# Kernel optimization log

Measured on AMD Instinct MI355X. Metric: run time of the kernel, lower is better.

## Reference

```python
import jax, jax.numpy as jnp
import numpy as np

BETA = 0.25
EPS = 1e-12

def setup_inputs() -> dict:
    key = jax.random.key(0)
    k1, k2 = jax.random.split(key)
    f_BChw = jax.random.normal(k1, (32, 64, 32, 32), dtype=jnp.float32)
    emb_weight = jax.random.normal(k2, (8192, 64), dtype=jnp.float32)
    return {"f_BChw": f_BChw, "emb_weight": emb_weight}

def reference(f_BChw, emb_weight):
    f = f_BChw.astype(jnp.float32)
    B, C, h, w = f.shape
    V = emb_weight.shape[0]
    # flatten tokens: [B,C,h,w] -> [N,C]
    NxC = jnp.transpose(f, (0, 2, 3, 1)).reshape(-1, C)
    # cosine nearest-neighbor on detached, L2-normalized queries/codes
    q = jax.lax.stop_gradient(NxC)
    q = q / jnp.maximum(jnp.linalg.norm(q, axis=-1, keepdims=True), EPS)
    wn = emb_weight / jnp.maximum(jnp.linalg.norm(emb_weight, axis=-1, keepdims=True), EPS)
    sim = q @ wn.T                      # [N,V] -- dominant memory traffic
    idx_N = jnp.argmax(sim, axis=1)     # [N]
    # gather codes -> [B,C,h,w]
    fhat = emb_weight[idx_N].reshape(B, h, w, C).transpose(0, 3, 1, 2)
    sg = jax.lax.stop_gradient
    vq_loss = BETA * jnp.mean((sg(fhat) - f) ** 2) + jnp.mean((fhat - sg(f)) ** 2)
    # straight-through estimator
    fhat_out = f + sg(fhat - f)
    # usage statistics (bincount)
    counts = jnp.zeros((V,), jnp.float32).at[idx_N].add(1.0)
    prob = counts / counts.sum()
    vocab_usage = jnp.mean((prob > 0.01 / V).astype(jnp.float32)) * 100.0
    entropy_loss = jnp.float32(0.0)
    return fhat_out, vq_loss, entropy_loss, vocab_usage
```

## Files before the change

kernel.cpp:

```cpp
#include <hip/hip_runtime.h>

typedef _Float16 f16x8 __attribute__((ext_vector_type(8)));
typedef float f32x16 __attribute__((ext_vector_type(16)));

#define V_TOTAL 8192
#define C_DIM   64
#define N_TOK   32768
#define INV2048 4.8828125e-4f
#define THR_COEF 2.2e-3f

#define VSPLIT1 4
#define VSEG1   2048
#define CH1     32
#define VSPLIT2 8
#define VSEG2   1024
#define CH2     32

typedef const __attribute__((address_space(1))) _Float16 glb_f16;
typedef __attribute__((address_space(3))) _Float16 lds_f16;


__device__ __forceinline__ unsigned long long packkey(float s, int idx) {
    unsigned u = __float_as_uint(s);
    unsigned k = u ^ ((unsigned)(((int)u) >> 31) | 0x80000000u);
    return ((unsigned long long)k << 32) | (unsigned)(8191 - idx);
}

__global__ __launch_bounds__(256)
void k_prep(const float* __restrict__ w, _Float16* __restrict__ cp,
            unsigned long long* __restrict__ keys, int* __restrict__ counts,
            int* __restrict__ unc_cnt) {
    int v = blockIdx.x * 256 + threadIdx.x;
    counts[v] = 0;
    if (v == 0) unc_cnt[0] = 0;
#pragma unroll
    for (int i = 0; i < 4; ++i) keys[v * 4 + i] = 0ull;
    const float4* row = (const float4*)(w + v * C_DIM);
    float4 r[16];
    float s = 0.f;
#pragma unroll
    for (int i = 0; i < 16; ++i) {
        r[i] = row[i];
        s += r[i].x * r[i].x + r[i].y * r[i].y + r[i].z * r[i].z + r[i].w * r[i].w;
    }
    float inv = 1.0f / fmaxf(sqrtf(s), 1e-12f);
    const float* rs = (const float*)r;
    const int cv = v >> 5, c = v & 31;
#pragma unroll
    for (int q = 0; q < 8; ++q) {
        f16x8 hi, lo;
#pragma unroll
        for (int j = 0; j < 8; ++j) {
            float x = rs[q * 8 + j] * inv;
            _Float16 h = (_Float16)x;
            hi[j] = h;
            lo[j] = (_Float16)((x - (float)h) * 2048.0f);
        }
        *(f16x8*)(cp + cv * 4096 +        q * 256 + c * 8) = hi;
        *(f16x8*)(cp + cv * 4096 + 2048 + q * 256 + c * 8) = lo;
    }
}

__global__ __launch_bounds__(256, 4)
void k_pass1(const float* __restrict__ f, const _Float16* __restrict__ cp,
             float* __restrict__ m1s, float* __restrict__ m2s,
             int* __restrict__ i1s, float* __restrict__ fn2) {
    __shared__ __align__(16) _Float16 lds[4][4096];

    const int tid  = threadIdx.x;
    const int lane = tid & 63;
    const int wid  = tid >> 6;
    const int c31  = lane & 31;
    const int g    = lane >> 5;
    const int seg  = blockIdx.y;
    const int t0   = blockIdx.x * 128 + wid * 32;

    f16x8 bh[4];
    float s2 = 0.f;
    {
        const int T = t0 + c31;
        const float* fb = f + (T >> 10) * 65536 + (T & 1023);
#pragma unroll
        for (int ks = 0; ks < 4; ++ks) {
#pragma unroll
            for (int j = 0; j < 8; ++j) {
                float v = fb[(ks * 16 + g * 8 + j) * 1024];
                s2 += v * v;
                bh[ks][j] = (_Float16)v;
            }
        }
    }

    const _Float16* seg_cp = cp + (size_t)seg * (VSEG1 / 32) * 4096;

    auto stage = [&](int cv) {
        const _Float16* s0 = seg_cp + (2 * cv + 0) * 4096 + wid * 512 + lane * 8;
        const _Float16* s1 = seg_cp + (2 * cv + 1) * 4096 + wid * 512 + lane * 8;
        _Float16* d0 = &lds[cv & 3][wid * 512];
        _Float16* d1 = &lds[cv & 3][2048 + wid * 512];
        __builtin_amdgcn_global_load_lds((glb_f16*)s0, (lds_f16*)d0, 16, 0, 0);
        __builtin_amdgcn_global_load_lds((glb_f16*)s1, (lds_f16*)d1, 16, 0, 0);
    };

    const f32x16 zacc = {0.f,0.f,0.f,0.f,0.f,0.f,0.f,0.f,0.f,0.f,0.f,0.f,0.f,0.f,0.f,0.f};

    float m1 = -3.4e38f, m2 = -3.4e38f;
    int   i1 = 0;

    stage(0); stage(1); stage(2);

#pragma unroll 1
    for (int cv = 0; cv < CH1; ++cv) {
        if (cv < CH1 - 2)       asm volatile("s_waitcnt vmcnt(4)" ::: "memory");
        else if (cv == CH1 - 2) asm volatile("s_waitcnt vmcnt(2)" ::: "memory");
        else                    asm volatile("s_waitcnt vmcnt(0)" ::: "memory");
        __builtin_amdgcn_s_barrier();
        if (cv + 3 < CH1) stage(cv + 3);

        const _Float16* base = &lds[cv & 3][g * 256 + c31 * 8];
#pragma unroll
        for (int tile = 0; tile < 2; ++tile) {
            const _Float16* tb = base + tile * 2048;
            f16x8 A0 = *(const f16x8*)(tb);
            f16x8 A1 = *(const f16x8*)(tb + 512);
            f16x8 A2 = *(const f16x8*)(tb + 1024);
            f16x8 A3 = *(const f16x8*)(tb + 1536);
            f32x16 amA, amB;
            amA = __builtin_amdgcn_mfma_f32_32x32x16_f16(A0, bh[0], zacc, 0, 0, 0);
            amB = __builtin_amdgcn_mfma_f32_32x32x16_f16(A2, bh[2], zacc, 0, 0, 0);
            amA = __builtin_amdgcn_mfma_f32_32x32x16_f16(A1, bh[1], amA, 0, 0, 0);
            amB = __builtin_amdgcn_mfma_f32_32x32x16_f16(A3, bh[3], amB, 0, 0, 0);

            const int codebase = seg * VSEG1 + cv * 64 + tile * 32;
#pragma unroll
            for (int r = 0; r < 16; ++r) {
                const int codeq = codebase + (r & 3) + 8 * (r >> 2);
                float s = amA[r] + amB[r];
                float nm2 = __builtin_amdgcn_fmed3f(m1, m2, s);
                bool u = s > m1;
                i1 = u ? codeq : i1;
                m1 = fmaxf(m1, s);
                m2 = nm2;
            }
        }
    }

    i1 += 4 * g;
    {
        float om1 = __shfl_xor(m1, 32);
        float om2 = __shfl_xor(m2, 32);
        int   oi1 = __shfl_xor(i1, 32);
        float nm2 = fmaxf(fminf(m1, om1), fmaxf(m2, om2));
        bool rep = om1 > m1;
        i1 = rep ? oi1 : i1;
        m1 = fmaxf(m1, om1);
        m2 = nm2;
        float os2 = __shfl_xor(s2, 32);
        s2 += os2;
    }
    if (lane < 32) {
        const int t = t0 + c31;
        m1s[seg * N_TOK + t] = m1;
        m2s[seg * N_TOK + t] = m2;
        i1s[seg * N_TOK + t] = i1;
        fn2[t] = s2;
    }
}

__global__ __launch_bounds__(256)
void k_classify(const float* __restrict__ m1s, const float* __restrict__ m2s,
                const int* __restrict__ i1s, const float* __restrict__ fn2,
                int* __restrict__ idxf, int* __restrict__ unc_list,
                int* __restrict__ unc_cnt) {
    const int t = blockIdx.x * 256 + threadIdx.x;
    float a1 = m1s[t], a2 = m2s[t];
    int   ai = i1s[t];
#pragma unroll
    for (int s = 1; s < VSPLIT1; ++s) {
        float b1 = m1s[s * N_TOK + t];
        float b2 = m2s[s * N_TOK + t];
        int   bi = i1s[s * N_TOK + t];
        float na2 = fmaxf(fminf(a1, b1), fmaxf(a2, b2));
        bool rep = b1 > a1;
        ai = rep ? bi : ai;
        a1 = fmaxf(a1, b1);
        a2 = na2;
    }
    const float thr = THR_COEF * sqrtf(fn2[t]);
    if (a1 - a2 > thr) {
        idxf[t] = ai;
    } else {
        idxf[t] = -1;
        int pos = atomicAdd(unc_cnt, 1);
        unc_list[pos] = t;
    }
}

__global__ __launch_bounds__(64, 2)
void k_pass2(const float* __restrict__ f, const _Float16* __restrict__ cp,
             const int* __restrict__ unc_list, const int* __restrict__ unc_cnt,
             unsigned long long* __restrict__ keys) {
    const int lane = threadIdx.x;
    const int c31  = lane & 31;
    const int g    = lane >> 5;
    const int seg  = blockIdx.y;

    const int n = unc_cnt[0];
    const int ngroups = (n + 31) >> 5;
    const f32x16 zacc = {0.f,0.f,0.f,0.f,0.f,0.f,0.f,0.f,0.f,0.f,0.f,0.f,0.f,0.f,0.f,0.f};

    for (int grp = blockIdx.x; grp < ngroups; grp += 256) {
        int j = grp * 32 + c31;
        if (j >= n) j = n - 1;
        const int T = unc_list[j];

        f16x8 bhh[4], bll[4];
        {
            const float* fb = f + (T >> 10) * 65536 + (T & 1023);
#pragma unroll
            for (int ks = 0; ks < 4; ++ks) {
#pragma unroll
                for (int jj = 0; jj < 8; ++jj) {
                    float v = fb[(ks * 16 + g * 8 + jj) * 1024];
                    _Float16 h = (_Float16)v;
                    bhh[ks][jj] = h;
                    bll[ks][jj] = (_Float16)((v - (float)h) * 2048.0f);
                }
            }
        }

        float best = -3.4e38f;
        int   bidx = 0;

#pragma unroll 1
        for (int cv = 0; cv < CH2; ++cv) {
            const _Float16* Ab = cp + (size_t)(seg * 32 + cv) * 4096 + g * 256 + c31 * 8;
            f16x8 Ah0 = *(const f16x8*)(Ab);
            f16x8 Ah1 = *(const f16x8*)(Ab + 512);
            f16x8 Ah2 = *(const f16x8*)(Ab + 1024);
            f16x8 Ah3 = *(const f16x8*)(Ab + 1536);
            f16x8 Al0 = *(const f16x8*)(Ab + 2048);
            f16x8 Al1 = *(const f16x8*)(Ab + 2560);
            f16x8 Al2 = *(const f16x8*)(Ab + 3072);
            f16x8 Al3 = *(const f16x8*)(Ab + 3584);

            f32x16 amA, amB, acA, acB;
            amA = __builtin_amdgcn_mfma_f32_32x32x16_f16(Ah0, bhh[0], zacc, 0, 0, 0);
            amB = __builtin_amdgcn_mfma_f32_32x32x16_f16(Ah2, bhh[2], zacc, 0, 0, 0);
            acA = __builtin_amdgcn_mfma_f32_32x32x16_f16(Ah0, bll[0], zacc, 0, 0, 0);
            acB = __builtin_amdgcn_mfma_f32_32x32x16_f16(Ah2, bll[2], zacc, 0, 0, 0);
            amA = __builtin_amdgcn_mfma_f32_32x32x16_f16(Ah1, bhh[1], amA, 0, 0, 0);
            amB = __builtin_amdgcn_mfma_f32_32x32x16_f16(Ah3, bhh[3], amB, 0, 0, 0);
            acA = __builtin_amdgcn_mfma_f32_32x32x16_f16(Al0, bhh[0], acA, 0, 0, 0);
            acB = __builtin_amdgcn_mfma_f32_32x32x16_f16(Al2, bhh[2], acB, 0, 0, 0);
            acA = __builtin_amdgcn_mfma_f32_32x32x16_f16(Ah1, bll[1], acA, 0, 0, 0);
            acB = __builtin_amdgcn_mfma_f32_32x32x16_f16(Ah3, bll[3], acB, 0, 0, 0);
            acA = __builtin_amdgcn_mfma_f32_32x32x16_f16(Al1, bhh[1], acA, 0, 0, 0);
            acB = __builtin_amdgcn_mfma_f32_32x32x16_f16(Al3, bhh[3], acB, 0, 0, 0);

            const int codebase = seg * VSEG2 + cv * 32;
#pragma unroll
            for (int r = 0; r < 16; ++r) {
                const int codeq = codebase + (r & 3) + 8 * (r >> 2);
                float s = fmaf(acA[r] + acB[r], INV2048, amA[r] + amB[r]);
                bool u = s > best;
                best = u ? s : best;
                bidx = u ? codeq : bidx;
            }
        }

        bidx += 4 * g;
        {
            float ov = __shfl_xor(best, 32);
            int   oi = __shfl_xor(bidx, 32);
            if (ov > best || (ov == best && oi < bidx)) { best = ov; bidx = oi; }
        }
        if (lane < 32) {
            atomicMax(&keys[T], packkey(best, bidx));
        }
    }
}

__global__ __launch_bounds__(256)
void k_finalize(const float* __restrict__ f, const float* __restrict__ w,
                const unsigned long long* __restrict__ keys,
                const int* __restrict__ idxf,
                int* __restrict__ counts, float* __restrict__ blocksq,
                float* __restrict__ out) {
    const int tid = threadIdx.x;
    const int t   = blockIdx.x * 256 + tid;

    int bi = idxf[t];
    if (bi < 0) bi = 8191 - (int)(unsigned)(keys[t] & 0xFFFFFFFFull);
    atomicAdd(&counts[bi], 1);

    float4 cr[16];
    const float4* crow = (const float4*)(w + bi * C_DIM);
#pragma unroll
    for (int i = 0; i < 16; ++i) cr[i] = crow[i];
    const float* crs = (const float*)cr;

    const int bb = t >> 10;
    const int hw = t & 1023;
    const float* fb = f + bb * 65536 + hw;
    float*       ob = out + bb * 65536 + hw;

    float s = 0.f;
#pragma unroll
    for (int c = 0; c < C_DIM; ++c) {
        float fv = fb[c * 1024];
        float d  = crs[c] - fv;
        s += d * d;
        ob[c * 1024] = fv + d;
    }

    __shared__ float red[256];
    red[tid] = s;
    __syncthreads();
    for (int st = 128; st > 0; st >>= 1) {
        if (tid < st) red[tid] += red[tid + st];
        __syncthreads();
    }
    if (tid == 0) blocksq[blockIdx.x] = red[0];
}

__global__ __launch_bounds__(256)
void k_stats(const int* __restrict__ counts, const float* __restrict__ blocksq,
             float* __restrict__ out) {
    __shared__ float redf[256];
    __shared__ int   redi[256];
    const int tid = threadIdx.x;
    int used = 0;
    for (int v = tid; v < V_TOTAL; v += 256) used += (counts[v] > 0) ? 1 : 0;
    redi[tid] = used;
    redf[tid] = (tid < 128) ? blocksq[tid] : 0.f;
    __syncthreads();
    for (int st = 128; st > 0; st >>= 1) {
        if (tid < st) { redi[tid] += redi[tid + st]; redf[tid] += redf[tid + st]; }
        __syncthreads();
    }
    if (tid == 0) {
        float mse = redf[0] / 2097152.0f;
        out[2097152] = 0.25f * mse + mse;
        out[2097153] = 0.0f;
        out[2097154] = 100.0f * (float)redi[0] / 8192.0f;
    }
}

extern "C" void kernel_launch(void* const* d_in, const int* in_sizes, int n_in,
                              void* d_out, int out_size, void* d_ws, size_t ws_size,
                              hipStream_t stream) {
    const float* f = (const float*)d_in[0];
    const float* w = (const float*)d_in[1];
    float* out = (float*)d_out;
    float* ws  = (float*)d_ws;

    _Float16*           cp       = (_Float16*)ws;
    float*              m1s      = ws + 524288;
    float*              m2s      = ws + 655360;
    int*                i1s      = (int*)(ws + 786432);
    float*              fn2      = ws + 917504;
    unsigned long long* keys     = (unsigned long long*)(ws + 950272);
    int*                idxf     = (int*)(ws + 1015808);
    int*                unc_list = (int*)(ws + 1048576);
    int*                unc_cnt  = (int*)(ws + 1081344);
    int*                counts   = (int*)(ws + 1081408);
    float*              blocksq  = ws + 1089600;

    hipLaunchKernelGGL(k_prep, dim3(32), dim3(256), 0, stream,
                       w, cp, keys, counts, unc_cnt);
    hipLaunchKernelGGL(k_pass1, dim3(N_TOK / 128, VSPLIT1), dim3(256), 0, stream,
                       f, cp, m1s, m2s, i1s, fn2);
    hipLaunchKernelGGL(k_classify, dim3(N_TOK / 256), dim3(256), 0, stream,
                       m1s, m2s, i1s, fn2, idxf, unc_list, unc_cnt);
    hipLaunchKernelGGL(k_pass2, dim3(256, VSPLIT2), dim3(64), 0, stream,
                       f, cp, unc_list, unc_cnt, keys);
    hipLaunchKernelGGL(k_finalize, dim3(N_TOK / 256), dim3(256), 0, stream,
                       f, w, keys, idxf, counts, blocksq, out);
    hipLaunchKernelGGL(k_stats, dim3(1), dim3(256), 0, stream,
                       counts, blocksq, out);
}
```

Measured before the change: 126.3 us.

## Fuse classify and stats into last-block epilogues; skip top-2 update when tile cannot win

k_classify is folded into k_pass1: the last of the four V-split blocks for each token tile, found with a per-tile atomic counter, merges the partial top-2 results and writes the uncertain-token list using wave-ballot compaction. k_stats is folded into k_finalize through a last-block-done counter. Inside pass1 the two interleaved MFMA accumulator chains become one dependent chain, and the per-row top-2 update is skipped unless some lane's tile maximum beats its current second best. This removes two kernel launches and most of the compare work, at the cost of a serial MFMA dependency chain and extra fences and atomics.

```diff
diff --git a/kernel.cpp b/kernel.cpp
--- a/kernel.cpp
+++ b/kernel.cpp
@@ -29,10 +29,12 @@
 __global__ __launch_bounds__(256)
 void k_prep(const float* __restrict__ w, _Float16* __restrict__ cp,
             unsigned long long* __restrict__ keys, int* __restrict__ counts,
-            int* __restrict__ unc_cnt) {
+            int* __restrict__ unc_cnt, int* __restrict__ tile_cnt,
+            int* __restrict__ fin_cnt) {
     int v = blockIdx.x * 256 + threadIdx.x;
     counts[v] = 0;
-    if (v == 0) unc_cnt[0] = 0;
+    if (v < 256) tile_cnt[v] = 0;
+    if (v == 0) { unc_cnt[0] = 0; fin_cnt[0] = 0; }
 #pragma unroll
     for (int i = 0; i < 4; ++i) keys[v * 4 + i] = 0ull;
     const float4* row = (const float4*)(w + v * C_DIM);
@@ -64,8 +66,11 @@
 __global__ __launch_bounds__(256, 4)
 void k_pass1(const float* __restrict__ f, const _Float16* __restrict__ cp,
              float* __restrict__ m1s, float* __restrict__ m2s,
-             int* __restrict__ i1s, float* __restrict__ fn2) {
+             int* __restrict__ i1s, float* __restrict__ fn2,
+             int* __restrict__ idxf, int* __restrict__ unc_list,
+             int* __restrict__ unc_cnt, int* __restrict__ tile_cnt) {
     __shared__ __align__(16) _Float16 lds[4][4096];
+    __shared__ int sflag;
 
     const int tid  = threadIdx.x;
     const int lane = tid & 63;
@@ -125,22 +130,33 @@
             f16x8 A1 = *(const f16x8*)(tb + 512);
             f16x8 A2 = *(const f16x8*)(tb + 1024);
             f16x8 A3 = *(const f16x8*)(tb + 1536);
-            f32x16 amA, amB;
-            amA = __builtin_amdgcn_mfma_f32_32x32x16_f16(A0, bh[0], zacc, 0, 0, 0);
-            amB = __builtin_amdgcn_mfma_f32_32x32x16_f16(A2, bh[2], zacc, 0, 0, 0);
-            amA = __builtin_amdgcn_mfma_f32_32x32x16_f16(A1, bh[1], amA, 0, 0, 0);
-            amB = __builtin_amdgcn_mfma_f32_32x32x16_f16(A3, bh[3], amB, 0, 0, 0);
-
-            const int codebase = seg * VSEG1 + cv * 64 + tile * 32;
-#pragma unroll
-            for (int r = 0; r < 16; ++r) {
-                const int codeq = codebase + (r & 3) + 8 * (r >> 2);
-                float s = amA[r] + amB[r];
-                float nm2 = __builtin_amdgcn_fmed3f(m1, m2, s);
-                bool u = s > m1;
-                i1 = u ? codeq : i1;
-                m1 = fmaxf(m1, s);
-                m2 = nm2;
+            f32x16 acc;
+            acc = __builtin_amdgcn_mfma_f32_32x32x16_f16(A0, bh[0], zacc, 0, 0, 0);
+            acc = __builtin_amdgcn_mfma_f32_32x32x16_f16(A1, bh[1], acc, 0, 0, 0);
+            acc = __builtin_amdgcn_mfma_f32_32x32x16_f16(A2, bh[2], acc, 0, 0, 0);
+            acc = __builtin_amdgcn_mfma_f32_32x32x16_f16(A3, bh[3], acc, 0, 0, 0);
+
+            float x0 = fmaxf(fmaxf(acc[0],  acc[1]),  acc[2]);
+            float x1 = fmaxf(fmaxf(acc[3],  acc[4]),  acc[5]);
+            float x2 = fmaxf(fmaxf(acc[6],  acc[7]),  acc[8]);
+            float x3 = fmaxf(fmaxf(acc[9],  acc[10]), acc[11]);
+            float x4 = fmaxf(fmaxf(acc[12], acc[13]), acc[14]);
+            float y0 = fmaxf(fmaxf(x0, x1), x2);
+            float y1 = fmaxf(fmaxf(x3, x4), acc[15]);
+            float cmax = fmaxf(y0, y1);
+
+            if (__any(cmax > m2)) {
+                const int codebase = seg * VSEG1 + cv * 64 + tile * 32;
+#pragma unroll
+                for (int r = 0; r < 16; ++r) {
+                    const int codeq = codebase + (r & 3) + 8 * (r >> 2);
+                    float s = acc[r];
+                    float nm2 = __builtin_amdgcn_fmed3f(m1, m2, s);
+                    bool u = s > m1;
+                    i1 = u ? codeq : i1;
+                    m1 = fmaxf(m1, s);
+                    m2 = nm2;
+                }
             }
         }
     }
@@ -155,8 +171,7 @@
         i1 = rep ? oi1 : i1;
         m1 = fmaxf(m1, om1);
         m2 = nm2;
-        float os2 = __shfl_xor(s2, 32);
-        s2 += os2;
+        s2 += __shfl_xor(s2, 32);
     }
     if (lane < 32) {
         const int t = t0 + c31;
@@ -165,34 +180,41 @@
         i1s[seg * N_TOK + t] = i1;
         fn2[t] = s2;
     }
-}
-
-__global__ __launch_bounds__(256)
-void k_classify(const float* __restrict__ m1s, const float* __restrict__ m2s,
-                const int* __restrict__ i1s, const float* __restrict__ fn2,
-                int* __restrict__ idxf, int* __restrict__ unc_list,
-                int* __restrict__ unc_cnt) {
-    const int t = blockIdx.x * 256 + threadIdx.x;
-    float a1 = m1s[t], a2 = m2s[t];
-    int   ai = i1s[t];
-#pragma unroll
-    for (int s = 1; s < VSPLIT1; ++s) {
-        float b1 = m1s[s * N_TOK + t];
-        float b2 = m2s[s * N_TOK + t];
-        int   bi = i1s[s * N_TOK + t];
-        float na2 = fmaxf(fminf(a1, b1), fmaxf(a2, b2));
-        bool rep = b1 > a1;
-        ai = rep ? bi : ai;
-        a1 = fmaxf(a1, b1);
-        a2 = na2;
-    }
-    const float thr = THR_COEF * sqrtf(fn2[t]);
-    if (a1 - a2 > thr) {
-        idxf[t] = ai;
-    } else {
-        idxf[t] = -1;
-        int pos = atomicAdd(unc_cnt, 1);
-        unc_list[pos] = t;
+
+    __syncthreads();
+    if (tid == 0) {
+        __threadfence();
+        int old = atomicAdd(&tile_cnt[blockIdx.x], 1);
+        sflag = (old == VSPLIT1 - 1) ? 1 : 0;
+    }
+    __syncthreads();
+    if (sflag && tid < 128) {
+        __threadfence();
+        const int t = blockIdx.x * 128 + tid;
+        float a1 = m1s[t], a2 = m2s[t];
+        int   ai = i1s[t];
+#pragma unroll
+        for (int s = 1; s < VSPLIT1; ++s) {
+            float b1 = m1s[s * N_TOK + t];
+            float b2 = m2s[s * N_TOK + t];
+            int   bi = i1s[s * N_TOK + t];
+            float na2 = fmaxf(fminf(a1, b1), fmaxf(a2, b2));
+            bool rep = b1 > a1;
+            ai = rep ? bi : ai;
+            a1 = fmaxf(a1, b1);
+            a2 = na2;
+        }
+        const float thr = THR_COEF * sqrtf(fn2[t]);
+        bool unc = !(a1 - a2 > thr);
+        idxf[t] = unc ? -1 : ai;
+        unsigned long long mask = __ballot(unc);
+        int l = tid & 63;
+        int prefix = __popcll(mask & ((1ull << l) - 1ull));
+        int total = __popcll(mask);
+        int base = 0;
+        if (l == 0 && total) base = atomicAdd(unc_cnt, total);
+        base = __shfl(base, 0);
+        if (unc) unc_list[base + prefix] = t;
     }
 }
 
@@ -286,7 +308,9 @@
                 const unsigned long long* __restrict__ keys,
                 const int* __restrict__ idxf,
                 int* __restrict__ counts, float* __restrict__ blocksq,
-                float* __restrict__ out) {
+                int* __restrict__ fin_cnt, float* __restrict__ out) {
+    __shared__ float red[256];
+    __shared__ int sflag;
     const int tid = threadIdx.x;
     const int t   = blockIdx.x * 256 + tid;
 
@@ -314,7 +338,6 @@
         ob[c * 1024] = fv + d;
     }
 
-    __shared__ float red[256];
     red[tid] = s;
     __syncthreads();
     for (int st = 128; st > 0; st >>= 1) {
@@ -322,28 +345,33 @@
         __syncthreads();
     }
     if (tid == 0) blocksq[blockIdx.x] = red[0];
-}
-
-__global__ __launch_bounds__(256)
-void k_stats(const int* __restrict__ counts, const float* __restrict__ blocksq,
-             float* __restrict__ out) {
-    __shared__ float redf[256];
-    __shared__ int   redi[256];
-    const int tid = threadIdx.x;
-    int used = 0;
-    for (int v = tid; v < V_TOTAL; v += 256) used += (counts[v] > 0) ? 1 : 0;
-    redi[tid] = used;
-    redf[tid] = (tid < 128) ? blocksq[tid] : 0.f;
+
+    if (tid == 0) {
+        __threadfence();
+        int old = atomicAdd(fin_cnt, 1);
+        sflag = (old == (int)gridDim.x - 1) ? 1 : 0;
+    }
     __syncthreads();
-    for (int st = 128; st > 0; st >>= 1) {
-        if (tid < st) { redi[tid] += redi[tid + st]; redf[tid] += redf[tid + st]; }
+    if (sflag) {
+        __threadfence();
+        __shared__ float redf[256];
+        __shared__ int   redi[256];
+        int used = 0;
+        for (int v = tid; v < V_TOTAL; v += 256) used += (counts[v] > 0) ? 1 : 0;
+        float bs = (tid < 128) ? blocksq[tid] : 0.f;
+        redi[tid] = used;
+        redf[tid] = bs;
         __syncthreads();
-    }
-    if (tid == 0) {
-        float mse = redf[0] / 2097152.0f;
-        out[2097152] = 0.25f * mse + mse;
-        out[2097153] = 0.0f;
-        out[2097154] = 100.0f * (float)redi[0] / 8192.0f;
+        for (int st = 128; st > 0; st >>= 1) {
+            if (tid < st) { redi[tid] += redi[tid + st]; redf[tid] += redf[tid + st]; }
+            __syncthreads();
+        }
+        if (tid == 0) {
+            float mse = redf[0] / 2097152.0f;
+            out[2097152] = 0.25f * mse + mse;
+            out[2097153] = 0.0f;
+            out[2097154] = 100.0f * (float)redi[0] / 8192.0f;
+        }
     }
 }
 
@@ -366,17 +394,15 @@
     int*                unc_cnt  = (int*)(ws + 1081344);
     int*                counts   = (int*)(ws + 1081408);
     float*              blocksq  = ws + 1089600;
+    int*                tile_cnt = (int*)(ws + 1089728);
+    int*                fin_cnt  = (int*)(ws + 1089984);
 
     hipLaunchKernelGGL(k_prep, dim3(32), dim3(256), 0, stream,
-                       w, cp, keys, counts, unc_cnt);
+                       w, cp, keys, counts, unc_cnt, tile_cnt, fin_cnt);
     hipLaunchKernelGGL(k_pass1, dim3(N_TOK / 128, VSPLIT1), dim3(256), 0, stream,
-                       f, cp, m1s, m2s, i1s, fn2);
-    hipLaunchKernelGGL(k_classify, dim3(N_TOK / 256), dim3(256), 0, stream,
-                       m1s, m2s, i1s, fn2, idxf, unc_list, unc_cnt);
+                       f, cp, m1s, m2s, i1s, fn2, idxf, unc_list, unc_cnt, tile_cnt);
     hipLaunchKernelGGL(k_pass2, dim3(256, VSPLIT2), dim3(64), 0, stream,
                        f, cp, unc_list, unc_cnt, keys);
     hipLaunchKernelGGL(k_finalize, dim3(N_TOK / 256), dim3(256), 0, stream,
-                       f, w, keys, idxf, counts, blocksq, out);
-    hipLaunchKernelGGL(k_stats, dim3(1), dim3(256), 0, stream,
-                       counts, blocksq, out);
-}
+                       f, w, keys, idxf, counts, blocksq, fin_cnt, out);
+}
```

Measured after the change: 158.6 us. 1.26x slower.
